# Optimization experiments

Measured on AMD Instinct MI355X. Metric: run time of the kernel, lower is better.

The kernel has to match this reference:

```python
import jax, jax.numpy as jnp
import numpy as np

B, S, H, NH = 2, 2048, 1024, 16
HD = H // NH  # 64
EPS = 1e-5


def setup_inputs() -> dict:
    key = jax.random.key(0)
    ks = jax.random.split(key, 4)
    return {
        "hidden_states": jax.random.normal(ks[0], (B, S, H), dtype=jnp.float32),
        "W_attn": jax.random.normal(ks[1], (H, 3 * H), dtype=jnp.float32) * (1.0 / np.sqrt(H)),
        "b_attn": jnp.zeros((3 * H,), dtype=jnp.float32),
        "W_proj": jax.random.normal(ks[2], (H, H), dtype=jnp.float32) * (1.0 / np.sqrt(H)),
        "b_proj": jnp.zeros((H,), dtype=jnp.float32),
        "q_gamma": jnp.ones((HD,), dtype=jnp.float32),
        "q_beta": jnp.zeros((HD,), dtype=jnp.float32),
        "k_gamma": jnp.ones((HD,), dtype=jnp.float32),
        "k_beta": jnp.zeros((HD,), dtype=jnp.float32),
    }


def _layernorm(x, gamma, beta):
    mu = jnp.mean(x, axis=-1, keepdims=True)
    var = jnp.mean(jnp.square(x - mu), axis=-1, keepdims=True)
    return (x - mu) * jax.lax.rsqrt(var + EPS) * gamma + beta


def reference(hidden_states, W_attn, b_attn, W_proj, b_proj, q_gamma, q_beta, k_gamma, k_beta):
    b, s, h = hidden_states.shape
    qkv = hidden_states @ W_attn + b_attn  # [B,S,3H]
    q, k, v = jnp.split(qkv, 3, axis=-1)
    # [B,S,H] -> [B,NH,S,HD]
    def to_heads(t):
        return t.reshape(b, s, NH, HD).transpose(0, 2, 1, 3)
    q, k, v = to_heads(q), to_heads(k), to_heads(v)
    # QK LayerNorm over head_dim
    q = _layernorm(q, q_gamma, q_beta)
    k = _layernorm(k, k_gamma, k_beta)
    scale = HD ** (-0.5)
    scores = jnp.einsum("bhqd,bhkd->bhqk", q, k) * scale
    causal = jnp.tril(jnp.ones((s, s), dtype=bool))
    mask_value = jnp.finfo(scores.dtype).min
    scores = jnp.where(causal, scores, mask_value)
    attn = jax.nn.softmax(scores.astype(jnp.float32), axis=-1).astype(q.dtype)
    out = jnp.einsum("bhqk,bhkd->bhqd", attn, v)
    out = out.transpose(0, 2, 1, 3).reshape(b, s, h)
    out = out @ W_proj + b_proj
    return out
```

## Files before the change

kernel.cpp:

```cpp
#include <hip/hip_runtime.h>
#include <hip/hip_bf16.h>

typedef __bf16 bf16x8 __attribute__((ext_vector_type(8)));
typedef float f32x4 __attribute__((ext_vector_type(4)));

#define EPS 1e-5f
#define QSCALE 0.18033688011112042f

__device__ __forceinline__ unsigned short f2bf(float f) {
  union { float f; unsigned int i; } c; c.f = f;
  unsigned int r = c.i + 0x7FFFu + ((c.i >> 16) & 1u);
  return (unsigned short)(r >> 16);
}

__global__ __launch_bounds__(256) void transpose_f32_bf16(
    const float* __restrict__ in, unsigned short* __restrict__ out,
    int R, int C)
{
  __shared__ __align__(16) unsigned short S[64 * 72];
  const int t = threadIdx.x;
  const int r = t >> 2, c4 = (t & 3) * 16;
  const int rt0 = blockIdx.y * 64, ct0 = blockIdx.x * 64;

  {
    long base = (long)(rt0 + r) * C + ct0 + c4;
    float4 a = *(const float4*)&in[base];
    float4 b = *(const float4*)&in[base + 4];
    float4 c = *(const float4*)&in[base + 8];
    float4 d = *(const float4*)&in[base + 12];
    unsigned short v[16] = {f2bf(a.x), f2bf(a.y), f2bf(a.z), f2bf(a.w),
                            f2bf(b.x), f2bf(b.y), f2bf(b.z), f2bf(b.w),
                            f2bf(c.x), f2bf(c.y), f2bf(c.z), f2bf(c.w),
                            f2bf(d.x), f2bf(d.y), f2bf(d.z), f2bf(d.w)};
    *(uint4*)&S[r * 72 + c4]     = *(uint4*)&v[0];
    *(uint4*)&S[r * 72 + c4 + 8] = *(uint4*)&v[8];
  }
  __syncthreads();

  unsigned short tmp[16];
#pragma unroll
  for (int j = 0; j < 16; j++) tmp[j] = S[(c4 + j) * 72 + r];
  *(uint4*)&out[(long)(ct0 + r) * R + rt0 + c4]     = *(uint4*)&tmp[0];
  *(uint4*)&out[(long)(ct0 + r) * R + rt0 + c4 + 8] = *(uint4*)&tmp[8];
}

__global__ __launch_bounds__(256) void convert_f32_bf16(
    const float* __restrict__ in, unsigned short* __restrict__ out)
{
  long i = ((long)blockIdx.x * 256 + threadIdx.x) * 16;
  float4 a = *(const float4*)&in[i];
  float4 b = *(const float4*)&in[i + 4];
  float4 c = *(const float4*)&in[i + 8];
  float4 d = *(const float4*)&in[i + 12];
  unsigned short v[16] = {f2bf(a.x), f2bf(a.y), f2bf(a.z), f2bf(a.w),
                          f2bf(b.x), f2bf(b.y), f2bf(b.z), f2bf(b.w),
                          f2bf(c.x), f2bf(c.y), f2bf(c.z), f2bf(c.w),
                          f2bf(d.x), f2bf(d.y), f2bf(d.z), f2bf(d.w)};
  *(uint4*)&out[i]     = *(uint4*)&v[0];
  *(uint4*)&out[i + 8] = *(uint4*)&v[8];
}

__global__ __launch_bounds__(256) void qkv_ln_kernel(
    const float* __restrict__ Xf,
    const unsigned short* __restrict__ Xbf, int use_xbf,
    const unsigned short* __restrict__ WT,
    const float* __restrict__ bias,
    const float* __restrict__ qg, const float* __restrict__ qb,
    const float* __restrict__ kg, const float* __restrict__ kb,
    unsigned short* __restrict__ Qws, unsigned short* __restrict__ Kws)
{
  __shared__ __align__(16) unsigned short As[2][128 * 32];
  __shared__ __align__(16) unsigned short Bs[2][128 * 32];

  const int tid = threadIdx.x;
  const int w = tid >> 6, lane = tid & 63, quad = lane >> 4, l15 = lane & 15;
  const int mh = w & 1, nh = w >> 1;
  const int n0 = blockIdx.x * 128, m0 = blockIdx.y * 128;

  f32x4 acc[4][4];
#pragma unroll
  for (int i = 0; i < 4; i++)
#pragma unroll
    for (int j = 0; j < 4; j++) acc[i][j] = (f32x4){0.f, 0.f, 0.f, 0.f};

  const int sr2 = tid >> 1, sh2 = (tid & 1) * 16;

  if (use_xbf) {
    long xo = (long)(m0 + sr2) * 1024 + sh2;
    *(uint4*)&As[0][sr2 * 32 + sh2]     = *(const uint4*)&Xbf[xo];
    *(uint4*)&As[0][sr2 * 32 + sh2 + 8] = *(const uint4*)&Xbf[xo + 8];
  } else {
    long xo = (long)(m0 + sr2) * 1024 + sh2;
    float4 a0 = *(const float4*)&Xf[xo];
    float4 a1 = *(const float4*)&Xf[xo + 4];
    float4 a2 = *(const float4*)&Xf[xo + 8];
    float4 a3 = *(const float4*)&Xf[xo + 12];
    unsigned short v[16] = {f2bf(a0.x), f2bf(a0.y), f2bf(a0.z), f2bf(a0.w),
                            f2bf(a1.x), f2bf(a1.y), f2bf(a1.z), f2bf(a1.w),
                            f2bf(a2.x), f2bf(a2.y), f2bf(a2.z), f2bf(a2.w),
                            f2bf(a3.x), f2bf(a3.y), f2bf(a3.z), f2bf(a3.w)};
    *(uint4*)&As[0][sr2 * 32 + sh2]     = *(uint4*)&v[0];
    *(uint4*)&As[0][sr2 * 32 + sh2 + 8] = *(uint4*)&v[8];
  }
  {
    long wo = (long)(n0 + sr2) * 1024 + sh2;
    *(uint4*)&Bs[0][sr2 * 32 + sh2]     = *(const uint4*)&WT[wo];
    *(uint4*)&Bs[0][sr2 * 32 + sh2 + 8] = *(const uint4*)&WT[wo + 8];
  }
  __syncthreads();

  int buf = 0;
  for (int kt = 0; kt < 1024; kt += 32) {
    const int nbuf = buf ^ 1;
    const bool pf = (kt + 32) < 1024;
    uint4 xv0, xv1, wv0, wv1;
    float4 a0, a1, a2, a3;
    if (pf) {
      if (use_xbf) {
        long xo = (long)(m0 + sr2) * 1024 + kt + 32 + sh2;
        xv0 = *(const uint4*)&Xbf[xo];
        xv1 = *(const uint4*)&Xbf[xo + 8];
      } else {
        long xo = (long)(m0 + sr2) * 1024 + kt + 32 + sh2;
        a0 = *(const float4*)&Xf[xo];
        a1 = *(const float4*)&Xf[xo + 4];
        a2 = *(const float4*)&Xf[xo + 8];
        a3 = *(const float4*)&Xf[xo + 12];
      }
      long wo = (long)(n0 + sr2) * 1024 + kt + 32 + sh2;
      wv0 = *(const uint4*)&WT[wo];
      wv1 = *(const uint4*)&WT[wo + 8];
    }

    bf16x8 af[4], bfr[4];
#pragma unroll
    for (int mq = 0; mq < 4; mq++)
      af[mq] = *(const bf16x8*)&As[buf][(mh * 64 + mq * 16 + l15) * 32 + quad * 8];
#pragma unroll
    for (int nq = 0; nq < 4; nq++)
      bfr[nq] = *(const bf16x8*)&Bs[buf][(nh * 64 + nq * 16 + l15) * 32 + quad * 8];
#pragma unroll
    for (int mq = 0; mq < 4; mq++)
#pragma unroll
      for (int nq = 0; nq < 4; nq++)
        acc[mq][nq] = __builtin_amdgcn_mfma_f32_16x16x32_bf16(af[mq], bfr[nq], acc[mq][nq], 0, 0, 0);

    if (pf) {
      if (use_xbf) {
        *(uint4*)&As[nbuf][sr2 * 32 + sh2]     = xv0;
        *(uint4*)&As[nbuf][sr2 * 32 + sh2 + 8] = xv1;
      } else {
        unsigned short v[16] = {f2bf(a0.x), f2bf(a0.y), f2bf(a0.z), f2bf(a0.w),
                                f2bf(a1.x), f2bf(a1.y), f2bf(a1.z), f2bf(a1.w),
                                f2bf(a2.x), f2bf(a2.y), f2bf(a2.z), f2bf(a2.w),
                                f2bf(a3.x), f2bf(a3.y), f2bf(a3.z), f2bf(a3.w)};
        *(uint4*)&As[nbuf][sr2 * 32 + sh2]     = *(uint4*)&v[0];
        *(uint4*)&As[nbuf][sr2 * 32 + sh2 + 8] = *(uint4*)&v[8];
      }
      *(uint4*)&Bs[nbuf][sr2 * 32 + sh2]     = wv0;
      *(uint4*)&Bs[nbuf][sr2 * 32 + sh2 + 8] = wv1;
    }
    __syncthreads();
    buf = nbuf;
  }

#pragma unroll
  for (int nq = 0; nq < 4; nq++) {
    float bv = bias[n0 + nh * 64 + nq * 16 + l15];
#pragma unroll
    for (int mq = 0; mq < 4; mq++)
#pragma unroll
      for (int rr = 0; rr < 4; rr++) acc[mq][nq][rr] += bv;
  }

  const int g = (n0 >> 6) + nh;
  const bool isQ = g < 16;

  {
    float gv[4], bev[4];
#pragma unroll
    for (int nq = 0; nq < 4; nq++) {
      int d = nq * 16 + l15;
      gv[nq]  = isQ ? qg[d] : kg[d];
      bev[nq] = isQ ? qb[d] : kb[d];
      if (isQ) { gv[nq] *= QSCALE; bev[nq] *= QSCALE; }
    }
#pragma unroll
    for (int mq = 0; mq < 4; mq++)
#pragma unroll
      for (int rr = 0; rr < 4; rr++) {
        float s  = acc[mq][0][rr] + acc[mq][1][rr] + acc[mq][2][rr] + acc[mq][3][rr];
        float s2 = acc[mq][0][rr]*acc[mq][0][rr] + acc[mq][1][rr]*acc[mq][1][rr]
                 + acc[mq][2][rr]*acc[mq][2][rr] + acc[mq][3][rr]*acc[mq][3][rr];
#pragma unroll
        for (int off = 1; off < 16; off <<= 1) {
          s  += __shfl_xor(s,  off, 64);
          s2 += __shfl_xor(s2, off, 64);
        }
        float mu   = s * (1.0f / 64.0f);
        float var  = fmaxf(s2 * (1.0f / 64.0f) - mu * mu, 0.f);
        float rstd = rsqrtf(var + EPS);
#pragma unroll
        for (int nq = 0; nq < 4; nq++)
          acc[mq][nq][rr] = (acc[mq][nq][rr] - mu) * rstd * gv[nq] + bev[nq];
      }
  }

  unsigned short* dst = isQ ? Qws : Kws;
  const int head = isQ ? g : g - 16;

#pragma unroll
  for (int mq = 0; mq < 4; mq++)
#pragma unroll
    for (int rr = 0; rr < 4; rr++) {
      int m = m0 + mh * 64 + mq * 16 + quad * 4 + rr;
      int b = m >> 11, s = m & 2047;
      long base = ((long)((b * 16 + head) * 2048 + s)) * 64;
#pragma unroll
      for (int nq = 0; nq < 4; nq++)
        dst[base + nq * 16 + l15] = f2bf(acc[mq][nq][rr]);
    }
}

__global__ __launch_bounds__(256) void vt_kernel(
    const float* __restrict__ Xf,
    const unsigned short* __restrict__ Xbf, int use_xbf,
    const unsigned short* __restrict__ WvT,
    const float* __restrict__ bias,
    unsigned short* __restrict__ Vt)
{
  __shared__ __align__(16) unsigned short As[2][128 * 32];
  __shared__ __align__(16) unsigned short Bs[2][64 * 32];

  const int tid = threadIdx.x;
  const int w = tid >> 6, lane = tid & 63, quad = lane >> 4, l15 = lane & 15;
  const int mh = w & 1, nh = w >> 1;
  const int n0 = blockIdx.x * 64, m0 = blockIdx.y * 128, bz = blockIdx.z;
  const long xrow0 = (long)bz * 2048;

  f32x4 acc[4][2];
#pragma unroll
  for (int i = 0; i < 4; i++)
#pragma unroll
    for (int j = 0; j < 2; j++) acc[i][j] = (f32x4){0.f, 0.f, 0.f, 0.f};

  const int srA = tid >> 1, shA = (tid & 1) * 16;
  const int srB = tid >> 2, shB = (tid & 3) * 8;

  {
    long wo = (long)(m0 + srA) * 1024 + shA;
    *(uint4*)&As[0][srA * 32 + shA]     = *(const uint4*)&WvT[wo];
    *(uint4*)&As[0][srA * 32 + shA + 8] = *(const uint4*)&WvT[wo + 8];
  }
  if (use_xbf) {
    long xo = (xrow0 + n0 + srB) * 1024 + shB;
    *(uint4*)&Bs[0][srB * 32 + shB] = *(const uint4*)&Xbf[xo];
  } else {
    long xo = (xrow0 + n0 + srB) * 1024 + shB;
    float4 a0 = *(const float4*)&Xf[xo];
    float4 a1 = *(const float4*)&Xf[xo + 4];
    unsigned short v[8] = {f2bf(a0.x), f2bf(a0.y), f2bf(a0.z), f2bf(a0.w),
                           f2bf(a1.x), f2bf(a1.y), f2bf(a1.z), f2bf(a1.w)};
    *(uint4*)&Bs[0][srB * 32 + shB] = *(uint4*)v;
  }
  __syncthreads();

  int buf = 0;
  for (int kt = 0; kt < 1024; kt += 32) {
    const int nbuf = buf ^ 1;
    const bool pf = (kt + 32) < 1024;
    uint4 wv0, wv1, xv0;
    float4 a0, a1;
    if (pf) {
      long wo = (long)(m0 + srA) * 1024 + kt + 32 + shA;
      wv0 = *(const uint4*)&WvT[wo];
      wv1 = *(const uint4*)&WvT[wo + 8];
      long xo = (xrow0 + n0 + srB) * 1024 + kt + 32 + shB;
      if (use_xbf) {
        xv0 = *(const uint4*)&Xbf[xo];
      } else {
        a0 = *(const float4*)&Xf[xo];
        a1 = *(const float4*)&Xf[xo + 4];
      }
    }

    bf16x8 af[4], bfr[2];
#pragma unroll
    for (int mq = 0; mq < 4; mq++)
      af[mq] = *(const bf16x8*)&As[buf][(mh * 64 + mq * 16 + l15) * 32 + quad * 8];
#pragma unroll
    for (int nq = 0; nq < 2; nq++)
      bfr[nq] = *(const bf16x8*)&Bs[buf][(nh * 32 + nq * 16 + l15) * 32 + quad * 8];
#pragma unroll
    for (int mq = 0; mq < 4; mq++)
#pragma unroll
      for (int nq = 0; nq < 2; nq++)
        acc[mq][nq] = __builtin_amdgcn_mfma_f32_16x16x32_bf16(af[mq], bfr[nq], acc[mq][nq], 0, 0, 0);

    if (pf) {
      *(uint4*)&As[nbuf][srA * 32 + shA]     = wv0;
      *(uint4*)&As[nbuf][srA * 32 + shA + 8] = wv1;
      if (use_xbf) {
        *(uint4*)&Bs[nbuf][srB * 32 + shB] = xv0;
      } else {
        unsigned short v[8] = {f2bf(a0.x), f2bf(a0.y), f2bf(a0.z), f2bf(a0.w),
                               f2bf(a1.x), f2bf(a1.y), f2bf(a1.z), f2bf(a1.w)};
        *(uint4*)&Bs[nbuf][srB * 32 + shB] = *(uint4*)v;
      }
    }
    __syncthreads();
    buf = nbuf;
  }

  const long outb = (long)bz * 2097152;
#pragma unroll
  for (int mq = 0; mq < 4; mq++)
#pragma unroll
    for (int rr = 0; rr < 4; rr++) {
      int m = m0 + mh * 64 + mq * 16 + quad * 4 + rr;
      float bv = bias[2048 + m];
#pragma unroll
      for (int nq = 0; nq < 2; nq++) {
        int n = n0 + nh * 32 + nq * 16 + l15;
        Vt[outb + (long)m * 2048 + n] = f2bf(acc[mq][nq][rr] + bv);
      }
    }
}

__global__ __launch_bounds__(256, 6) void attn_kernel(
    unsigned short* __restrict__ Qws,
    const unsigned short* __restrict__ Kws,
    const unsigned short* __restrict__ Vt)
{
  __shared__ __align__(16) unsigned short Ks[64 * 72];
  __shared__ __align__(16) unsigned short VTs[64 * 72];
  __shared__ __align__(16) unsigned short Ps[64 * 64];

  const int tid = threadIdx.x;
  const int w = tid >> 6, lane = tid & 63, quad = lane >> 4, l15 = lane & 15;
  const int bh = blockIdx.y;
  const int qt = ((bh >> 3) & 1) ? blockIdx.x : (31 - blockIdx.x);
  const int qbase = qt * 64;
  const long bhoff = (long)bh * 2048 * 64;
  const long bhv   = (long)bh * 131072;
  const int jmax = qt + 1;

  const int sr = tid >> 2, sc = (tid & 3) * 16;
  const int qsw = ((sr >> 2) & 3) << 4;

  *(uint4*)&Ps[sr * 64 + (sc ^ qsw)]       = *(const uint4*)&Qws[bhoff + (qbase + sr) * 64 + sc];
  *(uint4*)&Ps[sr * 64 + ((sc ^ qsw) + 8)] = *(const uint4*)&Qws[bhoff + (qbase + sr) * 64 + sc + 8];
  *(uint4*)&Ks[sr * 72 + sc]      = *(const uint4*)&Kws[bhoff + sr * 64 + sc];
  *(uint4*)&Ks[sr * 72 + sc + 8]  = *(const uint4*)&Kws[bhoff + sr * 64 + sc + 8];
  *(uint4*)&VTs[sr * 72 + sc]     = *(const uint4*)&Vt[bhv + sr * 2048 + sc];
  *(uint4*)&VTs[sr * 72 + sc + 8] = *(const uint4*)&Vt[bhv + sr * 2048 + sc + 8];
  __syncthreads();

  const int sw = ((l15 >> 2) & 3) << 4;
  const int pc0 = (quad * 8) ^ sw;
  const int pc1 = (32 + quad * 8) ^ sw;

  const bf16x8 qf0 = *(const bf16x8*)&Ps[(w * 16 + l15) * 64 + pc0];
  const bf16x8 qf1 = *(const bf16x8*)&Ps[(w * 16 + l15) * 64 + pc1];

  bf16x8 ones;
  {
    union { unsigned short u[8]; bf16x8 v; } c;
#pragma unroll
    for (int i = 0; i < 8; i++) c.u[i] = 0x3F80u;
    ones = c.v;
  }

  f32x4 o[4], osum;
#pragma unroll
  for (int i = 0; i < 4; i++) o[i] = (f32x4){0.f, 0.f, 0.f, 0.f};
  osum = (f32x4){0.f, 0.f, 0.f, 0.f};

  for (int j = 0; j < jmax; j++) {
    const int kb = j * 64;
    const bool pf = (j + 1) < jmax;
    uint4 pk0, pk1, pv0, pv1;
    if (pf) {
      const int kb1 = kb + 64;
      pk0 = *(const uint4*)&Kws[bhoff + (kb1 + sr) * 64 + sc];
      pk1 = *(const uint4*)&Kws[bhoff + (kb1 + sr) * 64 + sc + 8];
      pv0 = *(const uint4*)&Vt[bhv + sr * 2048 + kb1 + sc];
      pv1 = *(const uint4*)&Vt[bhv + sr * 2048 + kb1 + sc + 8];
    }

    f32x4 sacc[4];
#pragma unroll
    for (int i = 0; i < 4; i++) sacc[i] = (f32x4){0.f, 0.f, 0.f, 0.f};
#pragma unroll
    for (int nt = 0; nt < 4; nt++) {
      bf16x8 kf0 = *(const bf16x8*)&Ks[(nt * 16 + l15) * 72 + quad * 8];
      bf16x8 kf1 = *(const bf16x8*)&Ks[(nt * 16 + l15) * 72 + 32 + quad * 8];
      sacc[nt] = __builtin_amdgcn_mfma_f32_16x16x32_bf16(qf0, kf0, sacc[nt], 0, 0, 0);
      sacc[nt] = __builtin_amdgcn_mfma_f32_16x16x32_bf16(qf1, kf1, sacc[nt], 0, 0, 0);
    }

    const bool domask = (j == qt);
#pragma unroll
    for (int nt = 0; nt < 4; nt++)
#pragma unroll
      for (int rr = 0; rr < 4; rr++) {
        float p = exp2f(sacc[nt][rr]);
        if (domask) {
          int kcol = kb + nt * 16 + l15;
          int qrow = qbase + w * 16 + quad * 4 + rr;
          if (kcol > qrow) p = 0.f;
        }
        sacc[nt][rr] = p;
      }

#pragma unroll
    for (int rr = 0; rr < 4; rr++)
#pragma unroll
      for (int nt = 0; nt < 4; nt++)
        Ps[(w * 16 + quad * 4 + rr) * 64 + (((nt ^ quad) & 3) * 16 + l15)]
            = f2bf(sacc[nt][rr]);

    bf16x8 pfr0 = *(const bf16x8*)&Ps[(w * 16 + l15) * 64 + pc0];
    bf16x8 pfr1 = *(const bf16x8*)&Ps[(w * 16 + l15) * 64 + pc1];

    osum = __builtin_amdgcn_mfma_f32_16x16x32_bf16(pfr0, ones, osum, 0, 0, 0);
    osum = __builtin_amdgcn_mfma_f32_16x16x32_bf16(pfr1, ones, osum, 0, 0, 0);
#pragma unroll
    for (int dt = 0; dt < 4; dt++) {
      bf16x8 vf0 = *(const bf16x8*)&VTs[(dt * 16 + l15) * 72 + quad * 8];
      bf16x8 vf1 = *(const bf16x8*)&VTs[(dt * 16 + l15) * 72 + 32 + quad * 8];
      o[dt] = __builtin_amdgcn_mfma_f32_16x16x32_bf16(pfr0, vf0, o[dt], 0, 0, 0);
      o[dt] = __builtin_amdgcn_mfma_f32_16x16x32_bf16(pfr1, vf1, o[dt], 0, 0, 0);
    }

    if (pf) {
      __syncthreads();
      *(uint4*)&Ks[sr * 72 + sc]      = pk0;
      *(uint4*)&Ks[sr * 72 + sc + 8]  = pk1;
      *(uint4*)&VTs[sr * 72 + sc]     = pv0;
      *(uint4*)&VTs[sr * 72 + sc + 8] = pv1;
      __syncthreads();
    }
  }

#pragma unroll
  for (int rr = 0; rr < 4; rr++) {
    float inv = 1.0f / osum[rr];
    int row = qbase + w * 16 + quad * 4 + rr;
    long base = bhoff + (long)row * 64;
#pragma unroll
    for (int dt = 0; dt < 4; dt++)
      Qws[base + dt * 16 + l15] = f2bf(o[dt][rr] * inv);
  }
}

__global__ __launch_bounds__(256) void proj_kernel(
    const unsigned short* __restrict__ AQ,
    const unsigned short* __restrict__ WT,
    const float* __restrict__ bias,
    float* __restrict__ Out)
{
  __shared__ __align__(16) unsigned short As[2][128 * 32];
  __shared__ __align__(16) unsigned short Bs[2][64 * 32];

  const int tid = threadIdx.x;
  const int w = tid >> 6, lane = tid & 63, quad = lane >> 4, l15 = lane & 15;
  const int mh = w & 1, nh = w >> 1;
  const int n0 = blockIdx.x * 64, m0 = blockIdx.y * 128;

  f32x4 acc[4][2];
#pragma unroll
  for (int i = 0; i < 4; i++)
#pragma unroll
    for (int j = 0; j < 2; j++) acc[i][j] = (f32x4){0.f, 0.f, 0.f, 0.f};

  const int srA = tid >> 1, shA = (tid & 1) * 16;
  const int srB = tid >> 2, shB = (tid & 3) * 8;
  const int m = m0 + srA, b = m >> 11, s = m & 2047;

  {
    const int h = shA >> 6, d = shA & 63;
    long ao = ((long)((b * 16 + h) * 2048 + s)) * 64 + d;
    *(uint4*)&As[0][srA * 32 + shA]     = *(const uint4*)&AQ[ao];
    *(uint4*)&As[0][srA * 32 + shA + 8] = *(const uint4*)&AQ[ao + 8];
    long wo = (long)(n0 + srB) * 1024 + shB;
    *(uint4*)&Bs[0][srB * 32 + shB] = *(const uint4*)&WT[wo];
  }
  __syncthreads();

  int buf = 0;
  for (int kt = 0; kt < 1024; kt += 32) {
    const int nbuf = buf ^ 1;
    const bool pf = (kt + 32) < 1024;
    uint4 av0, av1, wv0;
    if (pf) {
      const int k = kt + 32 + shA, h = k >> 6, d = k & 63;
      long ao = ((long)((b * 16 + h) * 2048 + s)) * 64 + d;
      av0 = *(const uint4*)&AQ[ao];
      av1 = *(const uint4*)&AQ[ao + 8];
      long wo = (long)(n0 + srB) * 1024 + kt + 32 + shB;
      wv0 = *(const uint4*)&WT[wo];
    }

    bf16x8 af[4], bfr[2];
#pragma unroll
    for (int mq = 0; mq < 4; mq++)
      af[mq] = *(const bf16x8*)&As[buf][(mh * 64 + mq * 16 + l15) * 32 + quad * 8];
#pragma unroll
    for (int nq = 0; nq < 2; nq++)
      bfr[nq] = *(const bf16x8*)&Bs[buf][(nh * 32 + nq * 16 + l15) * 32 + quad * 8];
#pragma unroll
    for (int mq = 0; mq < 4; mq++)
#pragma unroll
      for (int nq = 0; nq < 2; nq++)
        acc[mq][nq] = __builtin_amdgcn_mfma_f32_16x16x32_bf16(af[mq], bfr[nq], acc[mq][nq], 0, 0, 0);

    if (pf) {
      *(uint4*)&As[nbuf][srA * 32 + shA]     = av0;
      *(uint4*)&As[nbuf][srA * 32 + shA + 8] = av1;
      *(uint4*)&Bs[nbuf][srB * 32 + shB]     = wv0;
    }
    __syncthreads();
    buf = nbuf;
  }

#pragma unroll
  for (int nq = 0; nq < 2; nq++) {
    int n = n0 + nh * 32 + nq * 16 + l15;
    float bv = bias[n];
#pragma unroll
    for (int mq = 0; mq < 4; mq++)
#pragma unroll
      for (int rr = 0; rr < 4; rr++) {
        int mm = m0 + mh * 64 + mq * 16 + quad * 4 + rr;
        Out[(long)mm * 1024 + n] = acc[mq][nq][rr] + bv;
      }
  }
}

extern "C" void kernel_launch(void* const* d_in, const int* in_sizes, int n_in,
                              void* d_out, int out_size, void* d_ws, size_t ws_size,
                              hipStream_t stream) {
  const float* X  = (const float*)d_in[0];
  const float* Wa = (const float*)d_in[1];
  const float* ba = (const float*)d_in[2];
  const float* Wp = (const float*)d_in[3];
  const float* bp = (const float*)d_in[4];
  const float* qg = (const float*)d_in[5];
  const float* qb = (const float*)d_in[6];
  const float* kg = (const float*)d_in[7];
  const float* kb = (const float*)d_in[8];

  const long per = 2L * 16 * 2048 * 64;
  unsigned short* ws  = (unsigned short*)d_ws;
  unsigned short* Qws = ws;
  unsigned short* Kws = Qws + per;
  unsigned short* Vt  = Kws + per;

  const bool big = ws_size >= (size_t)(5L * per * 2);
  unsigned short *Xbf, *WaT, *WpT;
  if (big) {
    Xbf = Vt + per;
    WaT = Xbf + per;
    WpT = WaT + 3072L * 1024;
  } else {
    Xbf = Qws;
    WaT = Vt + per;
    WpT = WaT + 3072L * 1024;
  }
  unsigned short* WvT = WaT + 2048L * 1024;

  transpose_f32_bf16<<<dim3(48, 16), 256, 0, stream>>>(Wa, WaT, 1024, 3072);
  transpose_f32_bf16<<<dim3(16, 16), 256, 0, stream>>>(Wp, WpT, 1024, 1024);
  if (big) convert_f32_bf16<<<1024, 256, 0, stream>>>(X, Xbf);
  qkv_ln_kernel<<<dim3(16, 32), 256, 0, stream>>>(X, Xbf, big ? 1 : 0, WaT, ba,
                                                  qg, qb, kg, kb, Qws, Kws);
  vt_kernel<<<dim3(32, 8, 2), 256, 0, stream>>>(X, Xbf, big ? 1 : 0, WvT, ba, Vt);
  attn_kernel<<<dim3(32, 32), 256, 0, stream>>>(Qws, Kws, Vt);
  proj_kernel<<<dim3(16, 32), 256, 0, stream>>>(Qws, WpT, bp, (float*)d_out);
}
```

Baseline: 221.8 us.

## Pair causal query tiles per attention block and fuse prep kernels into one launch

The attention kernel now launches half as many blocks. Each block processes query tile x and then tile 31-x, so every block does the same causal workload instead of relying on grid ordering to balance long and short tiles. The launch-bounds occupancy hint of 6 is dropped. The two weight transposes and the input conversion are merged into a single prep kernel with block-index dispatch, which removes two launches. The trade-off is fewer resident attention blocks (512 on 256 CUs) with serial phases, which may lower latency hiding.

```diff
diff --git a/kernel.cpp b/kernel.cpp
--- a/kernel.cpp
+++ b/kernel.cpp
@@ -13,15 +13,12 @@
   return (unsigned short)(r >> 16);
 }
 
-__global__ __launch_bounds__(256) void transpose_f32_bf16(
+__device__ __forceinline__ void transpose_tile(
     const float* __restrict__ in, unsigned short* __restrict__ out,
-    int R, int C)
+    int R, int C, int ct0, int rt0, unsigned short* S )
 {
-  __shared__ __align__(16) unsigned short S[64 * 72];
   const int t = threadIdx.x;
   const int r = t >> 2, c4 = (t & 3) * 16;
-  const int rt0 = blockIdx.y * 64, ct0 = blockIdx.x * 64;
-
   {
     long base = (long)(rt0 + r) * C + ct0 + c4;
     float4 a = *(const float4*)&in[base];
@@ -36,7 +33,6 @@
     *(uint4*)&S[r * 72 + c4 + 8] = *(uint4*)&v[8];
   }
   __syncthreads();
-
   unsigned short tmp[16];
 #pragma unroll
   for (int j = 0; j < 16; j++) tmp[j] = S[(c4 + j) * 72 + r];
@@ -44,20 +40,32 @@
   *(uint4*)&out[(long)(ct0 + r) * R + rt0 + c4 + 8] = *(uint4*)&tmp[8];
 }
 
-__global__ __launch_bounds__(256) void convert_f32_bf16(
-    const float* __restrict__ in, unsigned short* __restrict__ out)
+__global__ __launch_bounds__(256) void prep_kernel(
+    const float* __restrict__ Wa, const float* __restrict__ Wp,
+    const float* __restrict__ X,
+    unsigned short* __restrict__ WaT, unsigned short* __restrict__ WpT,
+    unsigned short* __restrict__ Xbf)
 {
-  long i = ((long)blockIdx.x * 256 + threadIdx.x) * 16;
-  float4 a = *(const float4*)&in[i];
-  float4 b = *(const float4*)&in[i + 4];
-  float4 c = *(const float4*)&in[i + 8];
-  float4 d = *(const float4*)&in[i + 12];
-  unsigned short v[16] = {f2bf(a.x), f2bf(a.y), f2bf(a.z), f2bf(a.w),
-                          f2bf(b.x), f2bf(b.y), f2bf(b.z), f2bf(b.w),
-                          f2bf(c.x), f2bf(c.y), f2bf(c.z), f2bf(c.w),
-                          f2bf(d.x), f2bf(d.y), f2bf(d.z), f2bf(d.w)};
-  *(uint4*)&out[i]     = *(uint4*)&v[0];
-  *(uint4*)&out[i + 8] = *(uint4*)&v[8];
+  __shared__ __align__(16) unsigned short S[64 * 72];
+  const int id = blockIdx.x;
+  if (id < 768) {
+    transpose_tile(Wa, WaT, 1024, 3072, (id % 48) * 64, (id / 48) * 64, S);
+  } else if (id < 1024) {
+    const int i2 = id - 768;
+    transpose_tile(Wp, WpT, 1024, 1024, (i2 % 16) * 64, (i2 / 16) * 64, S);
+  } else {
+    long i = ((long)(id - 1024) * 256 + threadIdx.x) * 16;
+    float4 a = *(const float4*)&X[i];
+    float4 b = *(const float4*)&X[i + 4];
+    float4 c = *(const float4*)&X[i + 8];
+    float4 d = *(const float4*)&X[i + 12];
+    unsigned short v[16] = {f2bf(a.x), f2bf(a.y), f2bf(a.z), f2bf(a.w),
+                            f2bf(b.x), f2bf(b.y), f2bf(b.z), f2bf(b.w),
+                            f2bf(c.x), f2bf(c.y), f2bf(c.z), f2bf(c.w),
+                            f2bf(d.x), f2bf(d.y), f2bf(d.z), f2bf(d.w)};
+    *(uint4*)&Xbf[i]     = *(uint4*)&v[0];
+    *(uint4*)&Xbf[i + 8] = *(uint4*)&v[8];
+  }
 }
 
 __global__ __launch_bounds__(256) void qkv_ln_kernel(
@@ -327,7 +335,7 @@
     }
 }
 
-__global__ __launch_bounds__(256, 6) void attn_kernel(
+__global__ __launch_bounds__(256) void attn_kernel(
     unsigned short* __restrict__ Qws,
     const unsigned short* __restrict__ Kws,
     const unsigned short* __restrict__ Vt)
@@ -339,30 +347,15 @@
   const int tid = threadIdx.x;
   const int w = tid >> 6, lane = tid & 63, quad = lane >> 4, l15 = lane & 15;
   const int bh = blockIdx.y;
-  const int qt = ((bh >> 3) & 1) ? blockIdx.x : (31 - blockIdx.x);
-  const int qbase = qt * 64;
   const long bhoff = (long)bh * 2048 * 64;
   const long bhv   = (long)bh * 131072;
-  const int jmax = qt + 1;
 
   const int sr = tid >> 2, sc = (tid & 3) * 16;
   const int qsw = ((sr >> 2) & 3) << 4;
-
-  *(uint4*)&Ps[sr * 64 + (sc ^ qsw)]       = *(const uint4*)&Qws[bhoff + (qbase + sr) * 64 + sc];
-  *(uint4*)&Ps[sr * 64 + ((sc ^ qsw) + 8)] = *(const uint4*)&Qws[bhoff + (qbase + sr) * 64 + sc + 8];
-  *(uint4*)&Ks[sr * 72 + sc]      = *(const uint4*)&Kws[bhoff + sr * 64 + sc];
-  *(uint4*)&Ks[sr * 72 + sc + 8]  = *(const uint4*)&Kws[bhoff + sr * 64 + sc + 8];
-  *(uint4*)&VTs[sr * 72 + sc]     = *(const uint4*)&Vt[bhv + sr * 2048 + sc];
-  *(uint4*)&VTs[sr * 72 + sc + 8] = *(const uint4*)&Vt[bhv + sr * 2048 + sc + 8];
-  __syncthreads();
-
   const int sw = ((l15 >> 2) & 3) << 4;
   const int pc0 = (quad * 8) ^ sw;
   const int pc1 = (32 + quad * 8) ^ sw;
 
-  const bf16x8 qf0 = *(const bf16x8*)&Ps[(w * 16 + l15) * 64 + pc0];
-  const bf16x8 qf1 = *(const bf16x8*)&Ps[(w * 16 + l15) * 64 + pc1];
-
   bf16x8 ones;
   {
     union { unsigned short u[8]; bf16x8 v; } c;
@@ -371,86 +364,106 @@
     ones = c.v;
   }
 
-  f32x4 o[4], osum;
-#pragma unroll
-  for (int i = 0; i < 4; i++) o[i] = (f32x4){0.f, 0.f, 0.f, 0.f};
-  osum = (f32x4){0.f, 0.f, 0.f, 0.f};
-
-  for (int j = 0; j < jmax; j++) {
-    const int kb = j * 64;
-    const bool pf = (j + 1) < jmax;
-    uint4 pk0, pk1, pv0, pv1;
-    if (pf) {
-      const int kb1 = kb + 64;
-      pk0 = *(const uint4*)&Kws[bhoff + (kb1 + sr) * 64 + sc];
-      pk1 = *(const uint4*)&Kws[bhoff + (kb1 + sr) * 64 + sc + 8];
-      pv0 = *(const uint4*)&Vt[bhv + sr * 2048 + kb1 + sc];
-      pv1 = *(const uint4*)&Vt[bhv + sr * 2048 + kb1 + sc + 8];
-    }
-
-    f32x4 sacc[4];
-#pragma unroll
-    for (int i = 0; i < 4; i++) sacc[i] = (f32x4){0.f, 0.f, 0.f, 0.f};
-#pragma unroll
-    for (int nt = 0; nt < 4; nt++) {
-      bf16x8 kf0 = *(const bf16x8*)&Ks[(nt * 16 + l15) * 72 + quad * 8];
-      bf16x8 kf1 = *(const bf16x8*)&Ks[(nt * 16 + l15) * 72 + 32 + quad * 8];
-      sacc[nt] = __builtin_amdgcn_mfma_f32_16x16x32_bf16(qf0, kf0, sacc[nt], 0, 0, 0);
-      sacc[nt] = __builtin_amdgcn_mfma_f32_16x16x32_bf16(qf1, kf1, sacc[nt], 0, 0, 0);
-    }
-
-    const bool domask = (j == qt);
-#pragma unroll
-    for (int nt = 0; nt < 4; nt++)
-#pragma unroll
-      for (int rr = 0; rr < 4; rr++) {
-        float p = exp2f(sacc[nt][rr]);
-        if (domask) {
-          int kcol = kb + nt * 16 + l15;
-          int qrow = qbase + w * 16 + quad * 4 + rr;
-          if (kcol > qrow) p = 0.f;
+#pragma unroll
+  for (int ph = 0; ph < 2; ph++) {
+    const int qt = ph ? (31 - blockIdx.x) : blockIdx.x;
+    const int qbase = qt * 64;
+    const int jmax = qt + 1;
+
+    if (ph) __syncthreads();
+
+    *(uint4*)&Ps[sr * 64 + (sc ^ qsw)]       = *(const uint4*)&Qws[bhoff + (qbase + sr) * 64 + sc];
+    *(uint4*)&Ps[sr * 64 + ((sc ^ qsw) + 8)] = *(const uint4*)&Qws[bhoff + (qbase + sr) * 64 + sc + 8];
+    *(uint4*)&Ks[sr * 72 + sc]      = *(const uint4*)&Kws[bhoff + sr * 64 + sc];
+    *(uint4*)&Ks[sr * 72 + sc + 8]  = *(const uint4*)&Kws[bhoff + sr * 64 + sc + 8];
+    *(uint4*)&VTs[sr * 72 + sc]     = *(const uint4*)&Vt[bhv + sr * 2048 + sc];
+    *(uint4*)&VTs[sr * 72 + sc + 8] = *(const uint4*)&Vt[bhv + sr * 2048 + sc + 8];
+    __syncthreads();
+
+    const bf16x8 qf0 = *(const bf16x8*)&Ps[(w * 16 + l15) * 64 + pc0];
+    const bf16x8 qf1 = *(const bf16x8*)&Ps[(w * 16 + l15) * 64 + pc1];
+
+    f32x4 o[4], osum;
+#pragma unroll
+    for (int i = 0; i < 4; i++) o[i] = (f32x4){0.f, 0.f, 0.f, 0.f};
+    osum = (f32x4){0.f, 0.f, 0.f, 0.f};
+
+    for (int j = 0; j < jmax; j++) {
+      const int kb = j * 64;
+      const bool pf = (j + 1) < jmax;
+      uint4 pk0, pk1, pv0, pv1;
+      if (pf) {
+        const int kb1 = kb + 64;
+        pk0 = *(const uint4*)&Kws[bhoff + (kb1 + sr) * 64 + sc];
+        pk1 = *(const uint4*)&Kws[bhoff + (kb1 + sr) * 64 + sc + 8];
+        pv0 = *(const uint4*)&Vt[bhv + sr * 2048 + kb1 + sc];
+        pv1 = *(const uint4*)&Vt[bhv + sr * 2048 + kb1 + sc + 8];
+      }
+
+      f32x4 sacc[4];
+#pragma unroll
+      for (int i = 0; i < 4; i++) sacc[i] = (f32x4){0.f, 0.f, 0.f, 0.f};
+#pragma unroll
+      for (int nt = 0; nt < 4; nt++) {
+        bf16x8 kf0 = *(const bf16x8*)&Ks[(nt * 16 + l15) * 72 + quad * 8];
+        bf16x8 kf1 = *(const bf16x8*)&Ks[(nt * 16 + l15) * 72 + 32 + quad * 8];
+        sacc[nt] = __builtin_amdgcn_mfma_f32_16x16x32_bf16(qf0, kf0, sacc[nt], 0, 0, 0);
+        sacc[nt] = __builtin_amdgcn_mfma_f32_16x16x32_bf16(qf1, kf1, sacc[nt], 0, 0, 0);
+      }
+
+      const bool domask = (j == qt);
+#pragma unroll
+      for (int nt = 0; nt < 4; nt++)
+#pragma unroll
+        for (int rr = 0; rr < 4; rr++) {
+          float p = exp2f(sacc[nt][rr]);
+          if (domask) {
+            int kcol = kb + nt * 16 + l15;
+            int qrow = qbase + w * 16 + quad * 4 + rr;
+            if (kcol > qrow) p = 0.f;
+          }
+          sacc[nt][rr] = p;
         }
-        sacc[nt][rr] = p;
-      }
-
-#pragma unroll
-    for (int rr = 0; rr < 4; rr++)
-#pragma unroll
-      for (int nt = 0; nt < 4; nt++)
-        Ps[(w * 16 + quad * 4 + rr) * 64 + (((nt ^ quad) & 3) * 16 + l15)]
-            = f2bf(sacc[nt][rr]);
-
-    bf16x8 pfr0 = *(const bf16x8*)&Ps[(w * 16 + l15) * 64 + pc0];
-    bf16x8 pfr1 = *(const bf16x8*)&Ps[(w * 16 + l15) * 64 + pc1];
-
-    osum = __builtin_amdgcn_mfma_f32_16x16x32_bf16(pfr0, ones, osum, 0, 0, 0);
-    osum = __builtin_amdgcn_mfma_f32_16x16x32_bf16(pfr1, ones, osum, 0, 0, 0);
-#pragma unroll
-    for (int dt = 0; dt < 4; dt++) {
-      bf16x8 vf0 = *(const bf16x8*)&VTs[(dt * 16 + l15) * 72 + quad * 8];
-      bf16x8 vf1 = *(const bf16x8*)&VTs[(dt * 16 + l15) * 72 + 32 + quad * 8];
-      o[dt] = __builtin_amdgcn_mfma_f32_16x16x32_bf16(pfr0, vf0, o[dt], 0, 0, 0);
-      o[dt] = __builtin_amdgcn_mfma_f32_16x16x32_bf16(pfr1, vf1, o[dt], 0, 0, 0);
-    }
-
-    if (pf) {
-      __syncthreads();
-      *(uint4*)&Ks[sr * 72 + sc]      = pk0;
-      *(uint4*)&Ks[sr * 72 + sc + 8]  = pk1;
-      *(uint4*)&VTs[sr * 72 + sc]     = pv0;
-      *(uint4*)&VTs[sr * 72 + sc + 8] = pv1;
-      __syncthreads();
-    }
-  }
-
-#pragma unroll
-  for (int rr = 0; rr < 4; rr++) {
-    float inv = 1.0f / osum[rr];
-    int row = qbase + w * 16 + quad * 4 + rr;
-    long base = bhoff + (long)row * 64;
-#pragma unroll
-    for (int dt = 0; dt < 4; dt++)
-      Qws[base + dt * 16 + l15] = f2bf(o[dt][rr] * inv);
+
+#pragma unroll
+      for (int rr = 0; rr < 4; rr++)
+#pragma unroll
+        for (int nt = 0; nt < 4; nt++)
+          Ps[(w * 16 + quad * 4 + rr) * 64 + (((nt ^ quad) & 3) * 16 + l15)]
+              = f2bf(sacc[nt][rr]);
+
+      bf16x8 pfr0 = *(const bf16x8*)&Ps[(w * 16 + l15) * 64 + pc0];
+      bf16x8 pfr1 = *(const bf16x8*)&Ps[(w * 16 + l15) * 64 + pc1];
+
+      osum = __builtin_amdgcn_mfma_f32_16x16x32_bf16(pfr0, ones, osum, 0, 0, 0);
+      osum = __builtin_amdgcn_mfma_f32_16x16x32_bf16(pfr1, ones, osum, 0, 0, 0);
+#pragma unroll
+      for (int dt = 0; dt < 4; dt++) {
+        bf16x8 vf0 = *(const bf16x8*)&VTs[(dt * 16 + l15) * 72 + quad * 8];
+        bf16x8 vf1 = *(const bf16x8*)&VTs[(dt * 16 + l15) * 72 + 32 + quad * 8];
+        o[dt] = __builtin_amdgcn_mfma_f32_16x16x32_bf16(pfr0, vf0, o[dt], 0, 0, 0);
+        o[dt] = __builtin_amdgcn_mfma_f32_16x16x32_bf16(pfr1, vf1, o[dt], 0, 0, 0);
+      }
+
+      if (pf) {
+        __syncthreads();
+        *(uint4*)&Ks[sr * 72 + sc]      = pk0;
+        *(uint4*)&Ks[sr * 72 + sc + 8]  = pk1;
+        *(uint4*)&VTs[sr * 72 + sc]     = pv0;
+        *(uint4*)&VTs[sr * 72 + sc + 8] = pv1;
+        __syncthreads();
+      }
+    }
+
+#pragma unroll
+    for (int rr = 0; rr < 4; rr++) {
+      float inv = 1.0f / osum[rr];
+      int row = qbase + w * 16 + quad * 4 + rr;
+      long base = bhoff + (long)row * 64;
+#pragma unroll
+      for (int dt = 0; dt < 4; dt++)
+        Qws[base + dt * 16 + l15] = f2bf(o[dt][rr] * inv);
+    }
   }
 }
 
@@ -570,12 +583,10 @@
   }
   unsigned short* WvT = WaT + 2048L * 1024;
 
-  transpose_f32_bf16<<<dim3(48, 16), 256, 0, stream>>>(Wa, WaT, 1024, 3072);
-  transpose_f32_bf16<<<dim3(16, 16), 256, 0, stream>>>(Wp, WpT, 1024, 1024);
-  if (big) convert_f32_bf16<<<1024, 256, 0, stream>>>(X, Xbf);
+  prep_kernel<<<big ? 2048 : 1024, 256, 0, stream>>>(Wa, Wp, X, WaT, WpT, Xbf);
   qkv_ln_kernel<<<dim3(16, 32), 256, 0, stream>>>(X, Xbf, big ? 1 : 0, WaT, ba,
                                                   qg, qb, kg, kb, Qws, Kws);
   vt_kernel<<<dim3(32, 8, 2), 256, 0, stream>>>(X, Xbf, big ? 1 : 0, WvT, ba, Vt);
-  attn_kernel<<<dim3(32, 32), 256, 0, stream>>>(Qws, Kws, Vt);
+  attn_kernel<<<dim3(16, 32), 256, 0, stream>>>(Qws, Kws, Vt);
   proj_kernel<<<dim3(16, 32), 256, 0, stream>>>(Qws, WpT, bp, (float*)d_out);
 }
```

Result: faster. 208.8 us (-5.9%).
